# Performance work log

Hardware: AMD Instinct MI355X
Metric: run time of the kernel (lower is better)

Reference implementation:

```python
import jax, jax.numpy as jnp
import numpy as np

N = 50_000       # nodes
E = 1_600_000    # edges (avg degree 32)
F_IN = 128       # input features
H = 32           # hidden channels (both GCNConv layers)
C = 16           # num classes


def setup_inputs() -> dict:
    key = jax.random.key(0)
    ks = jax.random.split(key, 6)
    x = jax.random.normal(ks[0], (N, F_IN), dtype=jnp.float32)
    edge_index = jax.random.randint(ks[1], (2, E), 0, N, dtype=jnp.int32)
    W1 = jax.random.normal(ks[2], (F_IN, H), dtype=jnp.float32) / np.float32(np.sqrt(F_IN))
    b1 = jnp.zeros((H,), jnp.float32)
    W2 = jax.random.normal(ks[3], (H, H), dtype=jnp.float32) / np.float32(np.sqrt(H))
    b2 = jnp.zeros((H,), jnp.float32)
    Wc = jax.random.normal(ks[4], (H, C), dtype=jnp.float32) / np.float32(np.sqrt(H))
    bc = jnp.zeros((C,), jnp.float32)
    return {"x": x, "edge_index": edge_index, "W1": W1, "b1": b1,
            "W2": W2, "b2": b2, "Wc": Wc, "bc": bc}


def _gcn_conv(x, W, b, src, dst, deg_inv_sqrt, n):
    """PyG GCNConv: xW, then D^{-1/2}(A+I)D^{-1/2} aggregation, then bias.

    src/dst already include self-loops; deg_inv_sqrt precomputed on dst.
    """
    xw = x @ W                                   # [N, H]
    norm = deg_inv_sqrt[src] * deg_inv_sqrt[dst]  # [E+N]
    msg = xw[src] * norm[:, None]                # gather + scale, [E+N, H]
    out = jax.ops.segment_sum(msg, dst, num_segments=n)  # scatter-add
    return out + b


def reference(x, edge_index, W1, b1, W2, b2, Wc, bc):
    n = x.shape[0]
    loops = jnp.arange(n, dtype=edge_index.dtype)
    src = jnp.concatenate([edge_index[0], loops])  # add self-loops
    dst = jnp.concatenate([edge_index[1], loops])
    # degree over destination column (edge weight 1), as PyG gcn_norm does
    deg = jax.ops.segment_sum(jnp.ones_like(dst, dtype=x.dtype), dst, num_segments=n)
    deg_inv_sqrt = jnp.where(deg > 0, jax.lax.rsqrt(deg), 0.0)

    h = jnp.tanh(_gcn_conv(x, W1, b1, src, dst, deg_inv_sqrt, n))
    h = jnp.tanh(_gcn_conv(h, W2, b2, src, dst, deg_inv_sqrt, n))
    out = h @ Wc + bc
    return (out, h)
```

## Files before the change

kernel.cpp:

```cpp
#include <hip/hip_runtime.h>
#include <hip/hip_bf16.h>

#define NN 50000
#define EE 1600000
#define FIN 128
#define HH 32
#define CC 16
#define NB 782
#define NBLK 391
#define CHUNK 4096

typedef unsigned short u16;
typedef unsigned int u32;
typedef unsigned char u8;

__device__ __forceinline__ float bf2f(u16 u) {
    union { u32 i; float f; } v; v.i = ((u32)u) << 16; return v.f;
}
__device__ __forceinline__ u16 f2bf(float f) {
    union { float f; u32 i; } v; v.f = f;
    u32 x = v.i;
    return (u16)((x + 0x7fffu + ((x >> 16) & 1u)) >> 16);
}

__global__ __launch_bounds__(256) void k_place(const int* __restrict__ src, const int* __restrict__ dst,
                                               int* __restrict__ locT,
                                               u16* __restrict__ gsrc, u8* __restrict__ grel) {
    __shared__ int dst_s[CHUNK];
    __shared__ u16 s_src[CHUNK];
    __shared__ u8  s_rel[CHUNK];
    __shared__ int cur[NB];
    __shared__ int ps[256];
    const int tid = threadIdx.x, blk = blockIdx.x;
    const int e0 = blk * CHUNK;
    int cnt = EE - e0; if (cnt > CHUNK) cnt = CHUNK;

    const uint4* gd4 = (const uint4*)(dst + e0);
    for (int i = tid; i < cnt / 4; i += 256) ((uint4*)dst_s)[i] = gd4[i];
    for (int i = tid; i < NB; i += 256) cur[i] = 0;
    __syncthreads();

    for (int k = 0; k < CHUNK / 256; ++k) {
        int i = k * 256 + tid;
        if (i < cnt) atomicAdd(&cur[dst_s[i] >> 6], 1);
    }
    __syncthreads();

    const int bi = tid * 4;
    int v0 = 0, v1 = 0, v2 = 0, v3 = 0;
    if (bi < NB)     v0 = cur[bi];
    if (bi + 1 < NB) v1 = cur[bi + 1];
    if (bi + 2 < NB) v2 = cur[bi + 2];
    if (bi + 3 < NB) v3 = cur[bi + 3];
    ps[tid] = v0 + v1 + v2 + v3;
    __syncthreads();
    for (int off = 1; off < 256; off <<= 1) {
        int t = (tid >= off) ? ps[tid - off] : 0;
        __syncthreads();
        ps[tid] += t;
        __syncthreads();
    }
    int run = (tid == 0) ? 0 : ps[tid - 1];
    if (bi < NB)     { cur[bi] = run;     locT[(size_t)bi * NBLK + blk] = run;     run += v0; }
    if (bi + 1 < NB) { cur[bi + 1] = run; locT[(size_t)(bi + 1) * NBLK + blk] = run; run += v1; }
    if (bi + 2 < NB) { cur[bi + 2] = run; locT[(size_t)(bi + 2) * NBLK + blk] = run; run += v2; }
    if (bi + 3 < NB) { cur[bi + 3] = run; locT[(size_t)(bi + 3) * NBLK + blk] = run; run += v3; }
    if (tid == 255) locT[(size_t)NB * NBLK + blk] = ps[255];
    __syncthreads();

    for (int k = 0; k < CHUNK / 256; ++k) {
        int i = k * 256 + tid;
        if (i < cnt) {
            int d = dst_s[i];
            int pos = atomicAdd(&cur[d >> 6], 1);
            s_src[pos] = (u16)src[e0 + i];
            s_rel[pos] = (u8)(d & 63);
        }
    }
    __syncthreads();

    const uint4* ss = (const uint4*)s_src;
    uint4* gs = (uint4*)(gsrc + (size_t)blk * CHUNK);
    for (int i = tid; i < (cnt * 2) / 16; i += 256) gs[i] = ss[i];
    const uint4* sr = (const uint4*)s_rel;
    uint4* gr = (uint4*)(grel + (size_t)blk * CHUNK);
    for (int i = tid; i < cnt / 16; i += 256) gr[i] = sr[i];
}

__global__ __launch_bounds__(256) void k_btot(const int* __restrict__ locT, int* __restrict__ btot) {
    __shared__ int ps[256];
    const int cb = blockIdx.x;
    int s = 0;
    for (int b = threadIdx.x; b < NBLK; b += 256)
        s += locT[(size_t)(cb + 1) * NBLK + b] - locT[(size_t)cb * NBLK + b];
    ps[threadIdx.x] = s;
    __syncthreads();
    for (int off = 128; off > 0; off >>= 1) {
        if (threadIdx.x < off) ps[threadIdx.x] += ps[threadIdx.x + off];
        __syncthreads();
    }
    if (threadIdx.x == 0) btot[cb] = ps[0];
}

__global__ __launch_bounds__(1024) void k_cscan(const int* __restrict__ btot, int* __restrict__ cbase,
                                                int* __restrict__ rowptr,
                                                const u32* __restrict__ xw_words, int* __restrict__ flag) {
    __shared__ int ps[1024];
    __shared__ int cs;
    const int t = threadIdx.x;
    if (t == 0) cs = 0;
    __syncthreads();
    if (t < 512) {
        float v = fabsf(bf2f((u16)(xw_words[t] & 0xffffu)));
        if (v >= 6.0e-8f && v <= 64.0f) atomicAdd(&cs, 1);
    }
    int myv = (t < NB) ? btot[t] : 0;
    ps[t] = myv;
    __syncthreads();
    for (int off = 1; off < 1024; off <<= 1) {
        int v = (t >= off) ? ps[t - off] : 0;
        __syncthreads();
        ps[t] += v;
        __syncthreads();
    }
    if (t < NB) cbase[t] = ps[t] - myv;
    if (t == 0) {
        cbase[NB] = EE; rowptr[NN] = EE;
        *flag = (cs > 384) ? 1 : 0;
    }
}

__global__ __launch_bounds__(256) void k_fine(const int* __restrict__ locT, const int* __restrict__ cbase,
                                              const u16* __restrict__ gsrc, const u8* __restrict__ grel,
                                              int* __restrict__ rowptr, float* __restrict__ dis,
                                              u16* __restrict__ entries) {
    __shared__ int beg_s[NBLK];
    __shared__ int len_s[NBLK];
    __shared__ int ps[256];
    __shared__ int h[64];
    __shared__ int cur[64];
    const int tid = threadIdx.x, cb = blockIdx.x;

    for (int b = tid; b < NBLK; b += 256) {
        int beg = locT[(size_t)cb * NBLK + b];
        beg_s[b] = beg;
        len_s[b] = locT[(size_t)(cb + 1) * NBLK + b] - beg;
    }
    if (tid < 64) h[tid] = 0;
    __syncthreads();

    for (int b = tid; b < NBLK; b += 256) {
        int g0 = b * CHUNK + beg_s[b];
        int L = len_s[b];
        for (int j = 0; j < L; ++j) atomicAdd(&h[grel[g0 + j]], 1);
    }
    __syncthreads();

    const int node0 = cb * 64;
    const int base = cbase[cb];
    int myv = (tid < 64) ? h[tid] : 0;
    ps[tid] = (tid < 64) ? myv : 0;
    __syncthreads();
    for (int off = 1; off < 64; off <<= 1) {
        int v = (tid >= off && tid < 64) ? ps[tid - off] : 0;
        __syncthreads();
        if (tid < 64) ps[tid] += v;
        __syncthreads();
    }
    if (tid < 64) {
        int excl = ps[tid] - myv;
        int n = node0 + tid;
        cur[tid] = base + excl;
        if (n < NN) {
            rowptr[n] = base + excl;
            dis[n] = rsqrtf((float)myv + 1.0f);
        }
    }
    __syncthreads();

    for (int b = tid; b < NBLK; b += 256) {
        int g0 = b * CHUNK + beg_s[b];
        int L = len_s[b];
        for (int j = 0; j < L; ++j) {
            int g = g0 + j;
            int pos = atomicAdd(&cur[grel[g]], 1);
            entries[pos] = gsrc[g];
        }
    }
}

__global__ __launch_bounds__(256) void k_xw1(const void* __restrict__ xv, const void* __restrict__ W1v,
                                             const float* __restrict__ dis,
                                             const int* __restrict__ flag, u16* __restrict__ xwb) {
    __shared__ float wsm[FIN * HH];
    __shared__ float xs[128][33];
    const int f = *flag;
    const int tid = threadIdx.x;
    if (f) {
        const u16* W1 = (const u16*)W1v;
        for (int i = tid; i < FIN * HH; i += 256) wsm[i] = bf2f(W1[i]);
    } else {
        const float* W1 = (const float*)W1v;
        for (int i = tid; i < FIN * HH; i += 256) wsm[i] = W1[i];
    }
    const int n0 = blockIdx.x * 128;
    const int ct = tid & 7, rg = tid >> 3;
    const int lr = tid >> 1, lh = tid & 1;
    int ln = n0 + lr; if (ln >= NN) ln = NN - 1;
    float acc[4][4] = {};
    for (int kc = 0; kc < FIN; kc += 32) {
        __syncthreads();
        float* dq = &xs[lr][lh * 16];
        if (f) {
            const u16* lp = (const u16*)xv + (size_t)ln * FIN + lh * 16 + kc;
            uint4 a = *(const uint4*)lp;
            uint4 b = *(const uint4*)(lp + 8);
            u32 aw[4] = {a.x, a.y, a.z, a.w}, bw[4] = {b.x, b.y, b.z, b.w};
            #pragma unroll
            for (int i = 0; i < 4; ++i) {
                dq[2*i]     = bf2f((u16)(aw[i] & 0xffffu));
                dq[2*i+1]   = bf2f((u16)(aw[i] >> 16));
                dq[8+2*i]   = bf2f((u16)(bw[i] & 0xffffu));
                dq[8+2*i+1] = bf2f((u16)(bw[i] >> 16));
            }
        } else {
            const float* lp = (const float*)xv + (size_t)ln * FIN + lh * 16 + kc;
            #pragma unroll
            for (int i = 0; i < 4; ++i) {
                float4 t = *(const float4*)(lp + 4 * i);
                dq[4*i] = t.x; dq[4*i+1] = t.y; dq[4*i+2] = t.z; dq[4*i+3] = t.w;
            }
        }
        __syncthreads();
        #pragma unroll
        for (int k = 0; k < 32; ++k) {
            float4 wv = *(const float4*)&wsm[(kc + k) * HH + ct * 4];
            #pragma unroll
            for (int j = 0; j < 4; ++j) {
                float xvv = xs[rg * 4 + j][k];
                acc[j][0] = fmaf(xvv, wv.x, acc[j][0]);
                acc[j][1] = fmaf(xvv, wv.y, acc[j][1]);
                acc[j][2] = fmaf(xvv, wv.z, acc[j][2]);
                acc[j][3] = fmaf(xvv, wv.w, acc[j][3]);
            }
        }
    }
    #pragma unroll
    for (int j = 0; j < 4; ++j) {
        int n = n0 + rg * 4 + j;
        if (n < NN) {
            float dd = dis[n];
            ushort4 o;
            o.x = f2bf(dd * acc[j][0]); o.y = f2bf(dd * acc[j][1]);
            o.z = f2bf(dd * acc[j][2]); o.w = f2bf(dd * acc[j][3]);
            *(ushort4*)&xwb[(size_t)n * HH + ct * 4] = o;
        }
    }
}

__global__ __launch_bounds__(256) void k_xw2(const u16* __restrict__ h1, const void* __restrict__ W2v,
                                             const float* __restrict__ dis,
                                             const int* __restrict__ flag, u16* __restrict__ xwb) {
    __shared__ float wsm[HH * HH];
    __shared__ float xs[128][33];
    const int f = *flag;
    const int tid = threadIdx.x;
    if (f) {
        const u16* W2 = (const u16*)W2v;
        for (int i = tid; i < HH * HH; i += 256) wsm[i] = bf2f(W2[i]);
    } else {
        const float* W2 = (const float*)W2v;
        for (int i = tid; i < HH * HH; i += 256) wsm[i] = W2[i];
    }
    const int n0 = blockIdx.x * 128;
    const int lr = tid >> 1, lh = tid & 1;
    int ln = n0 + lr; if (ln >= NN) ln = NN - 1;
    const u16* lp = h1 + (size_t)ln * HH + lh * 16;
    uint4 a = *(const uint4*)lp;
    uint4 b = *(const uint4*)(lp + 8);
    float* dq = &xs[lr][lh * 16];
    u32 aw[4] = {a.x, a.y, a.z, a.w}, bw[4] = {b.x, b.y, b.z, b.w};
    #pragma unroll
    for (int i = 0; i < 4; ++i) {
        dq[2*i]     = bf2f((u16)(aw[i] & 0xffffu));
        dq[2*i+1]   = bf2f((u16)(aw[i] >> 16));
        dq[8+2*i]   = bf2f((u16)(bw[i] & 0xffffu));
        dq[8+2*i+1] = bf2f((u16)(bw[i] >> 16));
    }
    __syncthreads();
    const int ct = tid & 7, rg = tid >> 3;
    float acc[4][4] = {};
    #pragma unroll
    for (int k = 0; k < 32; ++k) {
        float4 wv = *(const float4*)&wsm[k * HH + ct * 4];
        #pragma unroll
        for (int j = 0; j < 4; ++j) {
            float xv = xs[rg * 4 + j][k];
            acc[j][0] = fmaf(xv, wv.x, acc[j][0]);
            acc[j][1] = fmaf(xv, wv.y, acc[j][1]);
            acc[j][2] = fmaf(xv, wv.z, acc[j][2]);
            acc[j][3] = fmaf(xv, wv.w, acc[j][3]);
        }
    }
    #pragma unroll
    for (int j = 0; j < 4; ++j) {
        int n = n0 + rg * 4 + j;
        if (n < NN) {
            float dd = dis[n];
            ushort4 o;
            o.x = f2bf(dd * acc[j][0]); o.y = f2bf(dd * acc[j][1]);
            o.z = f2bf(dd * acc[j][2]); o.w = f2bf(dd * acc[j][3]);
            *(ushort4*)&xwb[(size_t)n * HH + ct * 4] = o;
        }
    }
}

__global__ __launch_bounds__(256) void k_gather(const int* __restrict__ rowptr, const u16* __restrict__ entries,
                                                const u16* __restrict__ xws, const float* __restrict__ dis,
                                                const void* __restrict__ bv, const int* __restrict__ flag,
                                                int force16, u16* __restrict__ dst16, float* __restrict__ dst32,
                                                int do_cls, const void* __restrict__ Wcv,
                                                const void* __restrict__ bcv, void* __restrict__ outv) {
    __shared__ float hrow[16][32];
    __shared__ float wcs[HH * CC];
    __shared__ float bcs[CC];
    const int f = *flag;
    const int tid = threadIdx.x;
    if (do_cls) {
        if (f) {
            const u16* Wc = (const u16*)Wcv;
            for (int i = tid; i < HH * CC; i += 256) wcs[i] = bf2f(Wc[i]);
            if (tid < CC) bcs[tid] = bf2f(((const u16*)bcv)[tid]);
        } else {
            const float* Wc = (const float*)Wcv;
            for (int i = tid; i < HH * CC; i += 256) wcs[i] = Wc[i];
            if (tid < CC) bcs[tid] = ((const float*)bcv)[tid];
        }
    }
    const int nl = tid >> 4;
    const int g = blockIdx.x * 16 + nl;
    const int c0 = (tid & 15) * 2;
    float b0, b1;
    if (f) { b0 = bf2f(((const u16*)bv)[c0]); b1 = bf2f(((const u16*)bv)[c0 + 1]); }
    else   { b0 = ((const float*)bv)[c0];     b1 = ((const float*)bv)[c0 + 1]; }
    const int beg = rowptr[g], end = rowptr[g + 1];
    const float dd = dis[g];
    u32 sw = *(const u32*)&xws[(size_t)g * HH + c0];
    float aL0 = bf2f((u16)(sw & 0xffffu)), aH0 = bf2f((u16)(sw >> 16));
    float aL1 = 0.f, aH1 = 0.f, aL2 = 0.f, aH2 = 0.f, aL3 = 0.f, aH3 = 0.f;
    int i = beg;
    for (; i + 4 <= end; i += 4) {
        int s0 = entries[i], s1 = entries[i + 1], s2 = entries[i + 2], s3 = entries[i + 3];
        u32 w0 = *(const u32*)&xws[(size_t)s0 * HH + c0];
        u32 w1 = *(const u32*)&xws[(size_t)s1 * HH + c0];
        u32 w2 = *(const u32*)&xws[(size_t)s2 * HH + c0];
        u32 w3 = *(const u32*)&xws[(size_t)s3 * HH + c0];
        aL0 += bf2f((u16)(w0 & 0xffffu)); aH0 += bf2f((u16)(w0 >> 16));
        aL1 += bf2f((u16)(w1 & 0xffffu)); aH1 += bf2f((u16)(w1 >> 16));
        aL2 += bf2f((u16)(w2 & 0xffffu)); aH2 += bf2f((u16)(w2 >> 16));
        aL3 += bf2f((u16)(w3 & 0xffffu)); aH3 += bf2f((u16)(w3 >> 16));
    }
    for (; i < end; ++i) {
        int s = entries[i];
        u32 w = *(const u32*)&xws[(size_t)s * HH + c0];
        aL0 += bf2f((u16)(w & 0xffffu)); aH0 += bf2f((u16)(w >> 16));
    }
    float vLo = tanhf(fmaf(dd, (aL0 + aL1) + (aL2 + aL3), b0));
    float vHi = tanhf(fmaf(dd, (aH0 + aH1) + (aH2 + aH3), b1));
    size_t idx = (size_t)g * HH + c0;
    if (force16 | f) {
        u32 o = (u32)f2bf(vLo) | ((u32)f2bf(vHi) << 16);
        *(u32*)&dst16[idx] = o;
    } else {
        *(float2*)&dst32[idx] = make_float2(vLo, vHi);
    }
    if (do_cls) {
        hrow[nl][c0] = vLo; hrow[nl][c0 + 1] = vHi;
        __syncthreads();
        int cl = tid & 15;
        float acc = bcs[cl];
        #pragma unroll
        for (int k = 0; k < HH; ++k) acc = fmaf(hrow[nl][k], wcs[k * CC + cl], acc);
        size_t oi = (size_t)g * CC + cl;
        if (f) ((u16*)outv)[oi] = f2bf(acc);
        else   ((float*)outv)[oi] = acc;
    }
}

extern "C" void kernel_launch(void* const* d_in, const int* in_sizes, int n_in,
                              void* d_out, int out_size, void* d_ws, size_t ws_size,
                              hipStream_t stream) {
    const void* x  = d_in[0];
    const int*  ei = (const int*)d_in[1];
    const void* W1 = d_in[2];
    const void* b1 = d_in[3];
    const void* W2 = d_in[4];
    const void* b2 = d_in[5];
    const void* Wc = d_in[6];
    const void* bc = d_in[7];
    const int* srcv = ei;
    const int* dstv = ei + EE;

    char*  ws     = (char*)d_ws;
    int*   flag   = (int*)ws;
    int*   rowptr = (int*)(ws + 4096);
    float* dis    = (float*)(ws + 208896);
    int*   cbase  = (int*)(ws + 413696);
    int*   btot   = (int*)(ws + 417792);
    int*   locT   = (int*)(ws + 421888);
    u16*   xwb    = (u16*)(ws + 1646592);
    u16*   entries= (u16*)(ws + 4846592);

    u16*   gsrc = (u16*)d_out;
    u8*    grel = (u8*)d_out + (size_t)EE * 2;

    u16*   h1    = (u16*)d_out;
    u16*   h2_16 = (u16*)d_out + (size_t)NN * CC;
    float* h2_32 = (float*)d_out + (size_t)NN * CC;

    k_place<<<NBLK, 256, 0, stream>>>(srcv, dstv, locT, gsrc, grel);
    k_btot<<<NB, 256, 0, stream>>>(locT, btot);
    k_cscan<<<1, 1024, 0, stream>>>(btot, cbase, rowptr, (const u32*)x, flag);
    k_fine<<<NB, 256, 0, stream>>>(locT, cbase, gsrc, grel, rowptr, dis, entries);

    k_xw1<<<(NN + 127) / 128, 256, 0, stream>>>(x, W1, dis, flag, xwb);
    k_gather<<<NN / 16, 256, 0, stream>>>(rowptr, entries, xwb, dis, b1, flag,
                                          1, h1, (float*)nullptr,
                                          0, nullptr, nullptr, nullptr);

    k_xw2<<<(NN + 127) / 128, 256, 0, stream>>>(h1, W2, dis, flag, xwb);
    k_gather<<<NN / 16, 256, 0, stream>>>(rowptr, entries, xwb, dis, b2, flag,
                                          0, h2_16, h2_32,
                                          1, Wc, bc, d_out);
}
```

Before: 193.3 us.

## Stage bucketed edges in LDS for fine sort and vectorize neighbor index loads

```diff
diff --git a/kernel.cpp b/kernel.cpp
--- a/kernel.cpp
+++ b/kernel.cpp
@@ -7,8 +7,9 @@
 #define HH 32
 #define CC 16
 #define NB 782
-#define NBLK 391
-#define CHUNK 4096
+#define NBLK 782
+#define CHUNK 2048
+#define FCAP 3072
 
 typedef unsigned short u16;
 typedef unsigned int u32;
@@ -61,7 +62,7 @@
         __syncthreads();
     }
     int run = (tid == 0) ? 0 : ps[tid - 1];
-    if (bi < NB)     { cur[bi] = run;     locT[(size_t)bi * NBLK + blk] = run;     run += v0; }
+    if (bi < NB)     { cur[bi] = run;     locT[(size_t)bi * NBLK + blk] = run;       run += v0; }
     if (bi + 1 < NB) { cur[bi + 1] = run; locT[(size_t)(bi + 1) * NBLK + blk] = run; run += v1; }
     if (bi + 2 < NB) { cur[bi + 2] = run; locT[(size_t)(bi + 2) * NBLK + blk] = run; run += v2; }
     if (bi + 3 < NB) { cur[bi + 3] = run; locT[(size_t)(bi + 3) * NBLK + blk] = run; run += v3; }
@@ -135,29 +136,69 @@
                                               int* __restrict__ rowptr, float* __restrict__ dis,
                                               u16* __restrict__ entries) {
     __shared__ int beg_s[NBLK];
-    __shared__ int len_s[NBLK];
+    __shared__ int fo[NBLK + 1];
     __shared__ int ps[256];
     __shared__ int h[64];
     __shared__ int cur[64];
+    __shared__ u16 lsrc[FCAP];
+    __shared__ u8  lrel[FCAP];
+    __shared__ u16 lout[FCAP];
     const int tid = threadIdx.x, cb = blockIdx.x;
 
     for (int b = tid; b < NBLK; b += 256) {
         int beg = locT[(size_t)cb * NBLK + b];
         beg_s[b] = beg;
-        len_s[b] = locT[(size_t)(cb + 1) * NBLK + b] - beg;
+        fo[b] = locT[(size_t)(cb + 1) * NBLK + b] - beg;
     }
     if (tid < 64) h[tid] = 0;
     __syncthreads();
 
-    for (int b = tid; b < NBLK; b += 256) {
-        int g0 = b * CHUNK + beg_s[b];
-        int L = len_s[b];
-        for (int j = 0; j < L; ++j) atomicAdd(&h[grel[g0 + j]], 1);
-    }
-    __syncthreads();
-
-    const int node0 = cb * 64;
+    const int b0 = tid * 4;
+    int a0 = 0, a1 = 0, a2 = 0, a3 = 0;
+    if (b0 < NBLK)     a0 = fo[b0];
+    if (b0 + 1 < NBLK) a1 = fo[b0 + 1];
+    if (b0 + 2 < NBLK) a2 = fo[b0 + 2];
+    if (b0 + 3 < NBLK) a3 = fo[b0 + 3];
+    ps[tid] = a0 + a1 + a2 + a3;
+    __syncthreads();
+    for (int off = 1; off < 256; off <<= 1) {
+        int v = (tid >= off) ? ps[tid - off] : 0;
+        __syncthreads();
+        ps[tid] += v;
+        __syncthreads();
+    }
+    int run = (tid == 0) ? 0 : ps[tid - 1];
+    if (b0 < NBLK)     { fo[b0] = run;     run += a0; }
+    if (b0 + 1 < NBLK) { fo[b0 + 1] = run; run += a1; }
+    if (b0 + 2 < NBLK) { fo[b0 + 2] = run; run += a2; }
+    if (b0 + 3 < NBLK) { fo[b0 + 3] = run; run += a3; }
+    if (tid == 255) fo[NBLK] = ps[255];
+    __syncthreads();
+    const int T = fo[NBLK];
     const int base = cbase[cb];
+    const bool staged = (T <= FCAP);
+
+    if (staged) {
+        for (int b = tid; b < NBLK; b += 256) {
+            int g0 = b * CHUNK + beg_s[b];
+            int o = fo[b];
+            int L = fo[b + 1] - o;
+            for (int j = 0; j < L; ++j) {
+                u8 r = grel[g0 + j];
+                lrel[o + j] = r;
+                lsrc[o + j] = gsrc[g0 + j];
+                atomicAdd(&h[r], 1);
+            }
+        }
+    } else {
+        for (int b = tid; b < NBLK; b += 256) {
+            int g0 = b * CHUNK + beg_s[b];
+            int L = fo[b + 1] - fo[b];
+            for (int j = 0; j < L; ++j) atomicAdd(&h[grel[g0 + j]], 1);
+        }
+    }
+    __syncthreads();
+
     int myv = (tid < 64) ? h[tid] : 0;
     ps[tid] = (tid < 64) ? myv : 0;
     __syncthreads();
@@ -169,8 +210,8 @@
     }
     if (tid < 64) {
         int excl = ps[tid] - myv;
-        int n = node0 + tid;
-        cur[tid] = base + excl;
+        int n = cb * 64 + tid;
+        cur[tid] = staged ? excl : base + excl;
         if (n < NN) {
             rowptr[n] = base + excl;
             dis[n] = rsqrtf((float)myv + 1.0f);
@@ -178,13 +219,22 @@
     }
     __syncthreads();
 
-    for (int b = tid; b < NBLK; b += 256) {
-        int g0 = b * CHUNK + beg_s[b];
-        int L = len_s[b];
-        for (int j = 0; j < L; ++j) {
-            int g = g0 + j;
-            int pos = atomicAdd(&cur[grel[g]], 1);
-            entries[pos] = gsrc[g];
+    if (staged) {
+        for (int i = tid; i < T; i += 256) {
+            int pos = atomicAdd(&cur[lrel[i]], 1);
+            lout[pos] = lsrc[i];
+        }
+        __syncthreads();
+        for (int i = tid; i < T; i += 256) entries[base + i] = lout[i];
+    } else {
+        for (int b = tid; b < NBLK; b += 256) {
+            int g0 = b * CHUNK + beg_s[b];
+            int L = fo[b + 1] - fo[b];
+            for (int j = 0; j < L; ++j) {
+                int g = g0 + j;
+                int pos = atomicAdd(&cur[grel[g]], 1);
+                entries[pos] = gsrc[g];
+            }
         }
     }
 }
@@ -349,20 +399,23 @@
     float aL0 = bf2f((u16)(sw & 0xffffu)), aH0 = bf2f((u16)(sw >> 16));
     float aL1 = 0.f, aH1 = 0.f, aL2 = 0.f, aH2 = 0.f, aL3 = 0.f, aH3 = 0.f;
     int i = beg;
+    for (; i < end && (i & 3); ++i) {
+        u32 w = *(const u32*)&xws[(size_t)entries[i] * HH + c0];
+        aL0 += bf2f((u16)(w & 0xffffu)); aH0 += bf2f((u16)(w >> 16));
+    }
     for (; i + 4 <= end; i += 4) {
-        int s0 = entries[i], s1 = entries[i + 1], s2 = entries[i + 2], s3 = entries[i + 3];
-        u32 w0 = *(const u32*)&xws[(size_t)s0 * HH + c0];
-        u32 w1 = *(const u32*)&xws[(size_t)s1 * HH + c0];
-        u32 w2 = *(const u32*)&xws[(size_t)s2 * HH + c0];
-        u32 w3 = *(const u32*)&xws[(size_t)s3 * HH + c0];
+        ushort4 e4 = *(const ushort4*)&entries[i];
+        u32 w0 = *(const u32*)&xws[(size_t)e4.x * HH + c0];
+        u32 w1 = *(const u32*)&xws[(size_t)e4.y * HH + c0];
+        u32 w2 = *(const u32*)&xws[(size_t)e4.z * HH + c0];
+        u32 w3 = *(const u32*)&xws[(size_t)e4.w * HH + c0];
         aL0 += bf2f((u16)(w0 & 0xffffu)); aH0 += bf2f((u16)(w0 >> 16));
         aL1 += bf2f((u16)(w1 & 0xffffu)); aH1 += bf2f((u16)(w1 >> 16));
         aL2 += bf2f((u16)(w2 & 0xffffu)); aH2 += bf2f((u16)(w2 >> 16));
         aL3 += bf2f((u16)(w3 & 0xffffu)); aH3 += bf2f((u16)(w3 >> 16));
     }
     for (; i < end; ++i) {
-        int s = entries[i];
-        u32 w = *(const u32*)&xws[(size_t)s * HH + c0];
+        u32 w = *(const u32*)&xws[(size_t)entries[i] * HH + c0];
         aL0 += bf2f((u16)(w & 0xffffu)); aH0 += bf2f((u16)(w >> 16));
     }
     float vLo = tanhf(fmaf(dd, (aL0 + aL1) + (aL2 + aL3), b0));
@@ -408,8 +461,8 @@
     int*   cbase  = (int*)(ws + 413696);
     int*   btot   = (int*)(ws + 417792);
     int*   locT   = (int*)(ws + 421888);
-    u16*   xwb    = (u16*)(ws + 1646592);
-    u16*   entries= (u16*)(ws + 4846592);
+    u16*   xwb    = (u16*)(ws + 2871296);
+    u16*   entries= (u16*)(ws + 6071296);
 
     u16*   gsrc = (u16*)d_out;
     u8*    grel = (u8*)d_out + (size_t)EE * 2;
```

Result: no change. 191.8 us (-0.8%).
